# Performance work log

Hardware: AMD Instinct MI355X
Metric: run time of the kernel (lower is better)

Reference implementation:

```python
import jax, jax.numpy as jnp
import numpy as np

D_MODEL = 1024
D_HEAD = 64
MAX_REL = 8
B, T = 4, 4096


def setup_inputs() -> dict:
    key = jax.random.key(0)
    k1, k2, k3, k4, k5 = jax.random.split(key, 5)
    return {
        "x": jax.random.normal(k1, (B, T, D_MODEL), dtype=jnp.float32),
        "W_q": jax.random.normal(k2, (D_HEAD, D_MODEL), dtype=jnp.float32) * (1.0 / np.sqrt(D_MODEL)),
        "W_k": jax.random.normal(k3, (D_HEAD, D_MODEL), dtype=jnp.float32) * (1.0 / np.sqrt(D_MODEL)),
        "W_v": jax.random.normal(k4, (D_HEAD, D_MODEL), dtype=jnp.float32) * (1.0 / np.sqrt(D_MODEL)),
        "rel_emb": jax.random.normal(k5, (2 * MAX_REL + 1, 1), dtype=jnp.float32),
    }


def reference(x, W_q, W_k, W_v, rel_emb):
    Bb, Tt, _ = x.shape
    scale = jnp.sqrt(jnp.asarray(W_q.shape[0], dtype=x.dtype))
    # projections (Linear: x @ W.T)
    q = jnp.einsum("btd,hd->bth", x, W_q)
    k = jnp.einsum("btd,hd->bth", x, W_k)
    v = jnp.einsum("btd,hd->bth", x, W_v)
    scores = jnp.einsum("bth,bsh->bts", q, k) / scale  # [B,T,T]
    # relative position bias: rel_emb[clip(j-i, -M, M) + M]
    i_idx = jnp.arange(Tt)[:, None]
    j_idx = jnp.arange(Tt)[None, :]
    rel = jnp.clip(j_idx - i_idx, -MAX_REL, MAX_REL) + MAX_REL  # [T,T] int
    rel_bias = rel_emb[rel, 0]  # [T,T]
    scores = scores + rel_bias[None, :, :]
    causal = j_idx <= i_idx  # [T,T] lower-triangular
    scores = jnp.where(causal[None, :, :], scores, -jnp.inf)
    attn = jax.nn.softmax(scores, axis=-1)
    return jnp.einsum("bts,bsh->bth", attn, v)
```

## Files before the change

### kernel.cpp

```cpp
#include <hip/hip_runtime.h>
#include <hip/hip_bf16.h>

#define BT 4
#define TT 4096
#define DM 1024
#define DH 64
#define NRE 17
#define LOG2E 1.4426950408889634f

using bf16 = __hip_bfloat16;
typedef __attribute__((ext_vector_type(8))) short short8;
typedef __attribute__((ext_vector_type(4))) short short4v;
typedef __attribute__((ext_vector_type(4))) float float4v;

#define BC8(x) __builtin_bit_cast(short8, x)

static __device__ __forceinline__ short8 load8(const bf16* p) {
    return *reinterpret_cast<const short8*>(p);
}
static __device__ __forceinline__ short bfbits(float x) {
    return (short)__bfloat16_as_ushort(__float2bfloat16(x));
}
static __device__ __forceinline__ short8 pack8(float4v a, float4v b) {
    short8 r;
    r[0] = bfbits(a[0]); r[1] = bfbits(a[1]); r[2] = bfbits(a[2]); r[3] = bfbits(a[3]);
    r[4] = bfbits(b[0]); r[5] = bfbits(b[1]); r[6] = bfbits(b[2]); r[7] = bfbits(b[3]);
    return r;
}
static __device__ __forceinline__ void gload_lds16(const void* g, void* l) {
    __builtin_amdgcn_global_load_lds(
        (const __attribute__((address_space(1))) void*)g,
        (__attribute__((address_space(3))) void*)l, 16, 0, 0);
}
static __device__ __forceinline__ unsigned lds_addr(const void* p) {
    return (unsigned)(size_t)(const __attribute__((address_space(3))) void*)p;
}

#define DSR(dst, addr, off) \
    asm volatile("ds_read_b128 %0, %1 offset:" off : "=v"(dst) : "v"(addr))


__global__ __launch_bounds__(256) void w_prep(
    const float* __restrict__ Wq, const float* __restrict__ Wk,
    const float* __restrict__ Wv, bf16* __restrict__ Wswz)
{
    const unsigned g = blockIdx.x * 256 + threadIdx.x;
    const unsigned c    = g / 768;
    const unsigned rem  = g - c * 768;
    const unsigned pair = rem >> 3;
    const unsigned slot = rem & 7;
    const unsigned l    = slot ^ (pair & 7);
    const unsigned row  = 2 * pair + (l >> 2);
    const unsigned k    = 32 * c + (l & 3) * 8;
    const float* src = (row < 64) ? &Wq[(size_t)row * DM + k]
                     : (row < 128) ? &Wk[(size_t)(row - 64) * DM + k]
                                   : &Wv[(size_t)(row - 128) * DM + k];
    float4v a = *reinterpret_cast<const float4v*>(src);
    float4v b = *reinterpret_cast<const float4v*>(src + 4);
    *reinterpret_cast<short8*>(&Wswz[(size_t)g * 8]) = pack8(a, b);
}

__global__ __launch_bounds__(256, 2) void qkv_gemm(
    const float* __restrict__ x, const bf16* __restrict__ Wswz,
    bf16* __restrict__ Qb, bf16* __restrict__ Kswz, bf16* __restrict__ Vswz)
{
    __shared__ __align__(16) float xs[2][2048];
    __shared__ __align__(16) short Wls[2][12288];

    const int w    = threadIdx.x >> 6;
    const int lane = threadIdx.x & 63;
    const int quad = lane >> 4;
    const int l16  = lane & 15;
    const int half = w & 1;
    const int colh = w >> 1;
    const int row0 = blockIdx.x * 32;

    float4v acc[6];
#pragma unroll
    for (int i = 0; i < 6; i++) acc[i] = (float4v)(0.f);

    auto stage = [&](int c, int p) {
#pragma unroll
        for (int j = 0; j < 2; j++) {
            const int call = 2 * w + j;
            const int row  = 4 * call + (lane >> 4);
            const int pu   = lane & 15;
            const int gu   = (pu & 8) | ((pu ^ row) & 7);
            gload_lds16(&x[(size_t)(row0 + row) * DM + c * 64 + gu * 4],
                        &xs[p][call * 256]);
        }
#pragma unroll
        for (int j = 0; j < 6; j++) {
            const int call = 6 * w + j;
            gload_lds16(&Wswz[(size_t)(2 * c) * 6144 + call * 512 + lane * 8],
                        &Wls[p][call * 512]);
        }
    };

    const unsigned xlds = lds_addr(&xs[0][0]);
    const unsigned wlds = lds_addr(&Wls[0][0]);
    const int R        = 16 * half + l16;
    const int lo3_0    = (2 * quad)     ^ (R & 7);
    const int lo3_1    = (2 * quad + 1) ^ (R & 7);
    const int pairBase = 48 * colh + (l16 >> 1);
    const int physW    = ((l16 & 1) * 4 + quad) ^ ((l16 >> 1) & 7);

    stage(0, 0);

    for (int c = 0; c < 16; c++) {
        const int p = c & 1;
        __syncthreads();
        if (c + 1 < 16) stage(c + 1, p ^ 1);

        const unsigned xb  = xlds + (unsigned)(p * 8192) + R * 64 * 4;
        const unsigned xa0 = xb + lo3_0 * 16;
        const unsigned xa1 = xb + lo3_1 * 16;
        const unsigned wa  = wlds + (unsigned)(p * 24576) + pairBase * 128 + physW * 16;

        float4v x00, x01, x10, x11;
        float4v w00, w01, w02, w03, w04, w05, w10, w11, w12, w13, w14, w15;
        DSR(x00, xa0, "0");   DSR(x10, xa0, "128");
        DSR(x01, xa1, "0");   DSR(x11, xa1, "128");
        DSR(w00, wa, "0");     DSR(w01, wa, "1024");  DSR(w02, wa, "2048");
        DSR(w03, wa, "3072");  DSR(w04, wa, "4096");  DSR(w05, wa, "5120");
        DSR(w10, wa, "12288"); DSR(w11, wa, "13312"); DSR(w12, wa, "14336");
        DSR(w13, wa, "15360"); DSR(w14, wa, "16384"); DSR(w15, wa, "17408");
        asm volatile("s_waitcnt lgkmcnt(0)"
            : "+v"(x00), "+v"(x01), "+v"(x10), "+v"(x11),
              "+v"(w00), "+v"(w01), "+v"(w02), "+v"(w03), "+v"(w04), "+v"(w05),
              "+v"(w10), "+v"(w11), "+v"(w12), "+v"(w13), "+v"(w14), "+v"(w15));

        short8 a0 = pack8(x00, x01);
        short8 a1 = pack8(x10, x11);
        acc[0] = __builtin_amdgcn_mfma_f32_16x16x32_bf16(a0, BC8(w00), acc[0], 0, 0, 0);
        acc[1] = __builtin_amdgcn_mfma_f32_16x16x32_bf16(a0, BC8(w01), acc[1], 0, 0, 0);
        acc[2] = __builtin_amdgcn_mfma_f32_16x16x32_bf16(a0, BC8(w02), acc[2], 0, 0, 0);
        acc[3] = __builtin_amdgcn_mfma_f32_16x16x32_bf16(a0, BC8(w03), acc[3], 0, 0, 0);
        acc[4] = __builtin_amdgcn_mfma_f32_16x16x32_bf16(a0, BC8(w04), acc[4], 0, 0, 0);
        acc[5] = __builtin_amdgcn_mfma_f32_16x16x32_bf16(a0, BC8(w05), acc[5], 0, 0, 0);
        acc[0] = __builtin_amdgcn_mfma_f32_16x16x32_bf16(a1, BC8(w10), acc[0], 0, 0, 0);
        acc[1] = __builtin_amdgcn_mfma_f32_16x16x32_bf16(a1, BC8(w11), acc[1], 0, 0, 0);
        acc[2] = __builtin_amdgcn_mfma_f32_16x16x32_bf16(a1, BC8(w12), acc[2], 0, 0, 0);
        acc[3] = __builtin_amdgcn_mfma_f32_16x16x32_bf16(a1, BC8(w13), acc[3], 0, 0, 0);
        acc[4] = __builtin_amdgcn_mfma_f32_16x16x32_bf16(a1, BC8(w14), acc[4], 0, 0, 0);
        acc[5] = __builtin_amdgcn_mfma_f32_16x16x32_bf16(a1, BC8(w15), acc[5], 0, 0, 0);
    }

    __syncthreads();
    short* Kimg = (short*)&xs[0][0];
    short* Vimg = Kimg + 2048;
#pragma unroll
    for (int nt = 0; nt < 6; nt++) {
        const int cc = 96 * colh + 16 * nt + l16;
#pragma unroll
        for (int r = 0; r < 4; r++) {
            const int jl = 16 * half + 4 * quad + r;
            const short hb = bfbits(acc[nt][r]);
            if (cc < 64) {
                Qb[(size_t)(row0 + jl) * DH + cc] = __hip_bfloat16_raw{(unsigned short)hb};
            } else if (cc < 128) {
                const int k  = cc - 64;
                const int h  = k >> 5;
                const int q2 = (k & 31) >> 3;
                Kimg[((2 * half + h) * 64 + q2 * 16 + 4 * quad + r) * 8 + (k & 7)] = hb;
            } else {
                const int d  = cc - 128;
                const int dh = d >> 5;
                const int hi = (d >> 4) & 1;
                Vimg[((2 * half + dh) * 64 + quad * 16 + (d & 15)) * 8 + hi * 4 + r] = hb;
            }
        }
    }
    __syncthreads();
    {
        const int b_     = row0 >> 12;
        const int tile32 = (row0 & (TT - 1)) >> 5;
        const size_t base = ((size_t)(b_ * 512 + tile32 * 4)) * 512;
        const int u = threadIdx.x;
        *reinterpret_cast<short8*>(&Kswz[base + (size_t)u * 8]) =
            *reinterpret_cast<const short8*>(&Kimg[u * 8]);
        *reinterpret_cast<short8*>(&Vswz[base + (size_t)u * 8]) =
            *reinterpret_cast<const short8*>(&Vimg[u * 8]);
    }
}

__global__ __launch_bounds__(512, 2) void attn(
    const bf16* __restrict__ Qb, const bf16* __restrict__ Kswz,
    const bf16* __restrict__ Vswz, const float* __restrict__ rel,
    float* __restrict__ out)
{
    __shared__ __align__(16) short sbuf[65536];

    const int w     = threadIdx.x >> 6;
    const int lane  = threadIdx.x & 63;
    const int quad  = lane >> 4;
    const int l16   = lane & 15;
    const int batch = blockIdx.x & 3;
    const int pr    = blockIdx.x >> 2;

    const float SCL = 0.125f * LOG2E;
    float relreg = 0.f;
    if (lane < NRE) relreg = rel[lane] * LOG2E;
    const float rel0 = __shfl(relreg, 0, 64);

    const size_t bbase = (size_t)batch * TT;

    short* mybuf = &sbuf[w * 8192];
    const unsigned sbase = lds_addr(&sbuf[0]) + (unsigned)(w * 16384 + lane * 16);

    float* Osh = (float*)&sbuf[0];
    float* mM  = Osh + 8 * 32 * 68;
    float* lL  = mM + 256;

    auto stageKV = [&](int T, int p) {
        const size_t gb = ((size_t)(batch * 512 + T * 4)) * 512;
        short* dK = mybuf + p * 4096;
#pragma unroll
        for (int j = 0; j < 4; j++)
            gload_lds16(&Kswz[gb + j * 512 + lane * 8], dK + j * 512);
#pragma unroll
        for (int j = 0; j < 4; j++)
            gload_lds16(&Vswz[gb + j * 512 + lane * 8], dK + 2048 + j * 512);
    };

#pragma unroll 1
    for (int ph = 0; ph < 2; ph++) {
        const int t  = ph ? (127 - pr) : pr;
        const int q0 = 32 * t;

        short8 bq[2][2];
#pragma unroll
        for (int qh = 0; qh < 2; qh++) {
            const bf16* qp = &Qb[(bbase + q0 + 16 * qh + l16) * DH];
            bq[qh][0] = load8(qp + quad * 8);
            bq[qh][1] = load8(qp + 32 + quad * 8);
        }
        __builtin_amdgcn_s_waitcnt(0xF70);

        float4v o[2][4];
#pragma unroll
        for (int qh = 0; qh < 2; qh++)
#pragma unroll
            for (int dt = 0; dt < 4; dt++) o[qh][dt] = (float4v)(0.f);
        float m_st[2] = {-1e30f, -1e30f}, l_st[2] = {0.f, 0.f};

        const int cnt = (t >= w) ? (((t - w) >> 3) + 1) : 0;
        if (cnt > 0) stageKV(w, 0);

        for (int k = 0; k < cnt; k++) {
            const int T = w + 8 * k;
            const int p = k & 1;
            if (k + 1 < cnt) {
                stageKV(w + 8 * (k + 1), p ^ 1);
                __builtin_amdgcn_s_waitcnt(0xF78);
            } else {
                __builtin_amdgcn_s_waitcnt(0xF70);
            }

            const unsigned ab = sbase + (unsigned)(p * 8192);
            float4v kf0, kf1, kf2, kf3, vf0, vf1, vf2, vf3;
            DSR(kf0, ab, "0");    DSR(kf1, ab, "1024");
            DSR(kf2, ab, "2048"); DSR(kf3, ab, "3072");
            DSR(vf0, ab, "4096"); DSR(vf1, ab, "5120");
            DSR(vf2, ab, "6144"); DSR(vf3, ab, "7168");
            asm volatile("s_waitcnt lgkmcnt(0)"
                : "+v"(kf0), "+v"(kf1), "+v"(kf2), "+v"(kf3),
                  "+v"(vf0), "+v"(vf1), "+v"(vf2), "+v"(vf3));

            const int js = 32 * T;
#pragma unroll
            for (int qh = 0; qh < 2; qh++) {
                float4v st[2];
                st[0] = (float4v)(0.f); st[1] = (float4v)(0.f);
                st[0] = __builtin_amdgcn_mfma_f32_16x16x32_bf16(BC8(kf0), bq[qh][0], st[0], 0, 0, 0);
                st[0] = __builtin_amdgcn_mfma_f32_16x16x32_bf16(BC8(kf1), bq[qh][1], st[0], 0, 0, 0);
                st[1] = __builtin_amdgcn_mfma_f32_16x16x32_bf16(BC8(kf2), bq[qh][0], st[1], 0, 0, 0);
                st[1] = __builtin_amdgcn_mfma_f32_16x16x32_bf16(BC8(kf3), bq[qh][1], st[1], 0, 0, 0);

                const int i_row = q0 + 16 * qh + l16;
                float mcur = -1e30f;
                if (js + 40 <= q0 + 16 * qh) {
#pragma unroll
                    for (int n = 0; n < 2; n++)
#pragma unroll
                        for (int r = 0; r < 4; r++) {
                            float v = st[n][r] * SCL + rel0;
                            st[n][r] = v;
                            mcur = fmaxf(mcur, v);
                        }
                } else {
#pragma unroll
                    for (int n = 0; n < 2; n++) {
                        const int jb = js + 16 * n + 4 * quad;
#pragma unroll
                        for (int r = 0; r < 4; r++) {
                            const int d = jb + r - i_row;
                            int idx = d + 8;
                            idx = idx < 0 ? 0 : (idx > 16 ? 16 : idx);
                            float v = st[n][r] * SCL + __shfl(relreg, idx, 64);
                            v = (d > 0) ? -1e30f : v;
                            st[n][r] = v;
                            mcur = fmaxf(mcur, v);
                        }
                    }
                }

                mcur = fmaxf(mcur, __shfl_xor(mcur, 16, 64));
                mcur = fmaxf(mcur, __shfl_xor(mcur, 32, 64));

                const float mn = fmaxf(m_st[qh], mcur);
                const float alpha = exp2f(m_st[qh] - mn);
                m_st[qh] = mn;

                float lsum = 0.f;
                short4v pb[2];
#pragma unroll
                for (int n = 0; n < 2; n++)
#pragma unroll
                    for (int r = 0; r < 4; r++) {
                        const float e = exp2f(st[n][r] - mn);
                        lsum += e;
                        pb[n][r] = bfbits(e);
                    }
                lsum += __shfl_xor(lsum, 16, 64);
                lsum += __shfl_xor(lsum, 32, 64);
                l_st[qh] = l_st[qh] * alpha + lsum;

#pragma unroll
                for (int dt = 0; dt < 4; dt++)
#pragma unroll
                    for (int r = 0; r < 4; r++) o[qh][dt][r] *= alpha;

#pragma unroll
                for (int n = 0; n < 2; n++) {
#pragma unroll
                    for (int dh = 0; dh < 2; dh++) {
                        const short8 vs = BC8((dh == 0) ? ((n == 0) ? vf0 : vf2)
                                                        : ((n == 0) ? vf1 : vf3));
                        short4v lo, hi;
                        lo[0] = vs[0]; lo[1] = vs[1]; lo[2] = vs[2]; lo[3] = vs[3];
                        hi[0] = vs[4]; hi[1] = vs[5]; hi[2] = vs[6]; hi[3] = vs[7];
                        o[qh][2 * dh]     = __builtin_amdgcn_mfma_f32_16x16x16bf16_1k(lo, pb[n], o[qh][2 * dh], 0, 0, 0);
                        o[qh][2 * dh + 1] = __builtin_amdgcn_mfma_f32_16x16x16bf16_1k(hi, pb[n], o[qh][2 * dh + 1], 0, 0, 0);
                    }
                }
            }
        }

        __syncthreads();
#pragma unroll
        for (int qh = 0; qh < 2; qh++) {
            const int row = w * 32 + 16 * qh + l16;
            if (quad == 0) { mM[row] = m_st[qh]; lL[row] = l_st[qh]; }
#pragma unroll
            for (int dt = 0; dt < 4; dt++)
                *reinterpret_cast<float4v*>(&Osh[row * 68 + 16 * dt + 4 * quad]) = o[qh][dt];
        }
        __syncthreads();

        for (int idx = threadIdx.x; idx < 32 * 64; idx += 512) {
            const int row = idx >> 6;
            const int col = idx & 63;
            float M = mM[row];
#pragma unroll
            for (int s = 1; s < 8; s++) M = fmaxf(M, mM[s * 32 + row]);
            float L = 0.f, acc = 0.f;
#pragma unroll
            for (int s = 0; s < 8; s++) {
                const float e = exp2f(mM[s * 32 + row] - M);
                L   += lL[s * 32 + row] * e;
                acc += Osh[(s * 32 + row) * 68 + col] * e;
            }
            out[(bbase + q0 + row) * DH + col] = acc / L;
        }
        __syncthreads();
    }
}

extern "C" void kernel_launch(void* const* d_in, const int* in_sizes, int n_in,
                              void* d_out, int out_size, void* d_ws, size_t ws_size,
                              hipStream_t stream)
{
    const float* x   = (const float*)d_in[0];
    const float* Wq  = (const float*)d_in[1];
    const float* Wk  = (const float*)d_in[2];
    const float* Wv  = (const float*)d_in[3];
    const float* rel = (const float*)d_in[4];
    float* out = (float*)d_out;

    bf16* Qb   = (bf16*)d_ws;
    bf16* Kswz = Qb   + (size_t)BT * TT * DH;
    bf16* Vswz = Kswz + (size_t)BT * TT * DH;
    bf16* Wswz = Vswz + (size_t)BT * TT * DH;

    w_prep<<<96, 256, 0, stream>>>(Wq, Wk, Wv, Wswz);
    qkv_gemm<<<512, 256, 0, stream>>>(x, Wswz, Qb, Kswz, Vswz);
    attn<<<256, 512, 0, stream>>>(Qb, Kswz, Vswz, rel, out);
}
```

Measured before the change: 150.0 us.

## Use 16 waves per attention block with lazy rescaling and single-buffered KV

```diff
diff --git a/kernel.cpp b/kernel.cpp
--- a/kernel.cpp
+++ b/kernel.cpp
@@ -184,7 +184,7 @@
     }
 }
 
-__global__ __launch_bounds__(512, 2) void attn(
+__global__ __launch_bounds__(1024, 4) void attn(
     const bf16* __restrict__ Qb, const bf16* __restrict__ Kswz,
     const bf16* __restrict__ Vswz, const float* __restrict__ rel,
     float* __restrict__ out)
@@ -205,22 +205,21 @@
 
     const size_t bbase = (size_t)batch * TT;
 
-    short* mybuf = &sbuf[w * 8192];
-    const unsigned sbase = lds_addr(&sbuf[0]) + (unsigned)(w * 16384 + lane * 16);
+    short* mybuf = &sbuf[w * 4096];
+    const unsigned sbase = lds_addr(&sbuf[0]) + (unsigned)(w * 8192 + lane * 16);
 
     float* Osh = (float*)&sbuf[0];
     float* mM  = Osh + 8 * 32 * 68;
-    float* lL  = mM + 256;
-
-    auto stageKV = [&](int T, int p) {
+    float* lL  = mM + 512;
+
+    auto stageKV = [&](int T) {
         const size_t gb = ((size_t)(batch * 512 + T * 4)) * 512;
-        short* dK = mybuf + p * 4096;
 #pragma unroll
         for (int j = 0; j < 4; j++)
-            gload_lds16(&Kswz[gb + j * 512 + lane * 8], dK + j * 512);
+            gload_lds16(&Kswz[gb + j * 512 + lane * 8], mybuf + j * 512);
 #pragma unroll
         for (int j = 0; j < 4; j++)
-            gload_lds16(&Vswz[gb + j * 512 + lane * 8], dK + 2048 + j * 512);
+            gload_lds16(&Vswz[gb + j * 512 + lane * 8], mybuf + 2048 + j * 512);
     };
 
 #pragma unroll 1
@@ -244,38 +243,35 @@
             for (int dt = 0; dt < 4; dt++) o[qh][dt] = (float4v)(0.f);
         float m_st[2] = {-1e30f, -1e30f}, l_st[2] = {0.f, 0.f};
 
-        const int cnt = (t >= w) ? (((t - w) >> 3) + 1) : 0;
-        if (cnt > 0) stageKV(w, 0);
+        const int cnt = (t >= w) ? (((t - w) >> 4) + 1) : 0;
+        if (cnt > 0) stageKV(w);
 
         for (int k = 0; k < cnt; k++) {
-            const int T = w + 8 * k;
-            const int p = k & 1;
-            if (k + 1 < cnt) {
-                stageKV(w + 8 * (k + 1), p ^ 1);
-                __builtin_amdgcn_s_waitcnt(0xF78);
-            } else {
-                __builtin_amdgcn_s_waitcnt(0xF70);
-            }
-
-            const unsigned ab = sbase + (unsigned)(p * 8192);
+            const int T = w + 16 * k;
+            __builtin_amdgcn_s_waitcnt(0xF70);
+
             float4v kf0, kf1, kf2, kf3, vf0, vf1, vf2, vf3;
-            DSR(kf0, ab, "0");    DSR(kf1, ab, "1024");
-            DSR(kf2, ab, "2048"); DSR(kf3, ab, "3072");
-            DSR(vf0, ab, "4096"); DSR(vf1, ab, "5120");
-            DSR(vf2, ab, "6144"); DSR(vf3, ab, "7168");
+            DSR(kf0, sbase, "0");    DSR(kf1, sbase, "1024");
+            DSR(kf2, sbase, "2048"); DSR(kf3, sbase, "3072");
+            DSR(vf0, sbase, "4096"); DSR(vf1, sbase, "5120");
+            DSR(vf2, sbase, "6144"); DSR(vf3, sbase, "7168");
             asm volatile("s_waitcnt lgkmcnt(0)"
                 : "+v"(kf0), "+v"(kf1), "+v"(kf2), "+v"(kf3),
                   "+v"(vf0), "+v"(vf1), "+v"(vf2), "+v"(vf3));
 
+            if (k + 1 < cnt) stageKV(w + 16 * (k + 1));
+
             const int js = 32 * T;
 #pragma unroll
             for (int qh = 0; qh < 2; qh++) {
                 float4v st[2];
                 st[0] = (float4v)(0.f); st[1] = (float4v)(0.f);
+                __builtin_amdgcn_s_setprio(1);
                 st[0] = __builtin_amdgcn_mfma_f32_16x16x32_bf16(BC8(kf0), bq[qh][0], st[0], 0, 0, 0);
                 st[0] = __builtin_amdgcn_mfma_f32_16x16x32_bf16(BC8(kf1), bq[qh][1], st[0], 0, 0, 0);
                 st[1] = __builtin_amdgcn_mfma_f32_16x16x32_bf16(BC8(kf2), bq[qh][0], st[1], 0, 0, 0);
                 st[1] = __builtin_amdgcn_mfma_f32_16x16x32_bf16(BC8(kf3), bq[qh][1], st[1], 0, 0, 0);
+                __builtin_amdgcn_s_setprio(0);
 
                 const int i_row = q0 + 16 * qh + l16;
                 float mcur = -1e30f;
@@ -308,9 +304,17 @@
                 mcur = fmaxf(mcur, __shfl_xor(mcur, 16, 64));
                 mcur = fmaxf(mcur, __shfl_xor(mcur, 32, 64));
 
-                const float mn = fmaxf(m_st[qh], mcur);
-                const float alpha = exp2f(m_st[qh] - mn);
-                m_st[qh] = mn;
+                if (__any(mcur > m_st[qh] + 8.f)) {
+                    const float mn = fmaxf(m_st[qh], mcur);
+                    const float alpha = exp2f(m_st[qh] - mn);
+                    m_st[qh] = mn;
+                    l_st[qh] *= alpha;
+#pragma unroll
+                    for (int dt = 0; dt < 4; dt++)
+#pragma unroll
+                        for (int r = 0; r < 4; r++) o[qh][dt][r] *= alpha;
+                }
+                const float mn = m_st[qh];
 
                 float lsum = 0.f;
                 short4v pb[2];
@@ -324,13 +328,9 @@
                     }
                 lsum += __shfl_xor(lsum, 16, 64);
                 lsum += __shfl_xor(lsum, 32, 64);
-                l_st[qh] = l_st[qh] * alpha + lsum;
-
-#pragma unroll
-                for (int dt = 0; dt < 4; dt++)
-#pragma unroll
-                    for (int r = 0; r < 4; r++) o[qh][dt][r] *= alpha;
-
+                l_st[qh] += lsum;
+
+                __builtin_amdgcn_s_setprio(1);
 #pragma unroll
                 for (int n = 0; n < 2; n++) {
 #pragma unroll
@@ -344,6 +344,7 @@
                         o[qh][2 * dh + 1] = __builtin_amdgcn_mfma_f32_16x16x16bf16_1k(hi, pb[n], o[qh][2 * dh + 1], 0, 0, 0);
                     }
                 }
+                __builtin_amdgcn_s_setprio(0);
             }
         }
 
@@ -352,26 +353,62 @@
         for (int qh = 0; qh < 2; qh++) {
             const int row = w * 32 + 16 * qh + l16;
             if (quad == 0) { mM[row] = m_st[qh]; lL[row] = l_st[qh]; }
-#pragma unroll
-            for (int dt = 0; dt < 4; dt++)
-                *reinterpret_cast<float4v*>(&Osh[row * 68 + 16 * dt + 4 * quad]) = o[qh][dt];
-        }
-        __syncthreads();
-
-        for (int idx = threadIdx.x; idx < 32 * 64; idx += 512) {
-            const int row = idx >> 6;
-            const int col = idx & 63;
+        }
+        if (w < 8) {
+#pragma unroll
+            for (int qh = 0; qh < 2; qh++) {
+                const int row = w * 32 + 16 * qh + l16;
+#pragma unroll
+                for (int dt = 0; dt < 4; dt++)
+                    *reinterpret_cast<float4v*>(&Osh[row * 68 + 16 * dt + 4 * quad]) = o[qh][dt];
+            }
+        }
+        __syncthreads();
+
+        const int idx = threadIdx.x;
+        float Mv[2], Lv[2], av[2];
+#pragma unroll
+        for (int e = 0; e < 2; e++) {
+            const int row = (idx + e * 1024) >> 6;
             float M = mM[row];
 #pragma unroll
-            for (int s = 1; s < 8; s++) M = fmaxf(M, mM[s * 32 + row]);
-            float L = 0.f, acc = 0.f;
+            for (int s = 1; s < 16; s++) M = fmaxf(M, mM[s * 32 + row]);
+            Mv[e] = M;
+            float L = 0.f, a = 0.f;
+            const int col = (idx + e * 1024) & 63;
 #pragma unroll
             for (int s = 0; s < 8; s++) {
-                const float e = exp2f(mM[s * 32 + row] - M);
-                L   += lL[s * 32 + row] * e;
-                acc += Osh[(s * 32 + row) * 68 + col] * e;
-            }
-            out[(bbase + q0 + row) * DH + col] = acc / L;
+                const float ex = exp2f(mM[s * 32 + row] - M);
+                L += lL[s * 32 + row] * ex;
+                a += Osh[(s * 32 + row) * 68 + col] * ex;
+            }
+            Lv[e] = L; av[e] = a;
+        }
+        __syncthreads();
+
+        if (w >= 8) {
+#pragma unroll
+            for (int qh = 0; qh < 2; qh++) {
+                const int row = (w - 8) * 32 + 16 * qh + l16;
+#pragma unroll
+                for (int dt = 0; dt < 4; dt++)
+                    *reinterpret_cast<float4v*>(&Osh[row * 68 + 16 * dt + 4 * quad]) = o[qh][dt];
+            }
+        }
+        __syncthreads();
+
+#pragma unroll
+        for (int e = 0; e < 2; e++) {
+            const int row = (idx + e * 1024) >> 6;
+            const int col = (idx + e * 1024) & 63;
+            float L = Lv[e], a = av[e];
+#pragma unroll
+            for (int s = 8; s < 16; s++) {
+                const float ex = exp2f(mM[s * 32 + row] - Mv[e]);
+                L += lL[s * 32 + row] * ex;
+                a += Osh[((s - 8) * 32 + row) * 68 + col] * ex;
+            }
+            out[(bbase + q0 + row) * DH + col] = a / L;
         }
         __syncthreads();
     }
@@ -395,5 +432,5 @@
 
     w_prep<<<96, 256, 0, stream>>>(Wq, Wk, Wv, Wswz);
     qkv_gemm<<<512, 256, 0, stream>>>(x, Wswz, Qb, Kswz, Vswz);
-    attn<<<256, 512, 0, stream>>>(Qb, Kswz, Vswz, rel, out);
-}
+    attn<<<256, 1024, 0, stream>>>(Qb, Kswz, Vswz, rel, out);
+}
```

New measurement: 185.9 us. +23.9%, slower.
